# Kernel tuning notes

Hardware: AMD Instinct MI355X
Metric: run time of the kernel (lower is better)

Reference implementation:

```python
import jax, jax.numpy as jnp
import numpy as np
import math

FEATURE_DIM = 128
INPUT_DIM = 2
OUTPUT_DIM = 3
SIGMA_Q = 128.0
SIGMA_LS = [16.0, 64.0, 256.0]
N_PATCHES = 256
HIDDEN = 512
HEADS = 2
DIM_HEAD = 64
ALPHA = 10.0
N_FREQ = FEATURE_DIM // (2 * INPUT_DIM)  # 32
B, HW = 8, 16384


def _omegas(sigma):
    # torch.logspace(1, log10(sigma), n): 10^1 .. sigma, n points
    return jnp.logspace(1.0, math.log10(sigma), N_FREQ, dtype=jnp.float32)


def calc_gamma(coords, omegas):
    # coords: [L, D] -> [L, D*2*n]
    arg = jnp.pi * coords[:, :, None] * omegas[None, None, :]  # [L, D, n]
    g = jnp.concatenate([jnp.sin(arg), jnp.cos(arg)], axis=-1)  # [L, D, 2n]
    return g.reshape(coords.shape[0], -1)


def setup_inputs() -> dict:
    key = jax.random.key(0)
    ks = jax.random.split(key, 16)
    w = lambda k, shape: (jax.random.normal(k, shape, dtype=jnp.float32) * 0.05)
    return {
        "x": jax.random.uniform(ks[0], (B, HW, INPUT_DIM), dtype=jnp.float32),
        "tokens": jax.random.normal(ks[1], (B, N_PATCHES, HIDDEN), dtype=jnp.float32),
        "q_W": w(ks[2], (FEATURE_DIM, HIDDEN)),
        "q_b": w(ks[3], (HIDDEN,)),
        "Wq": w(ks[4], (HIDDEN, HEADS * DIM_HEAD)),
        "Wkv": w(ks[5], (HIDDEN, 2 * HEADS * DIM_HEAD)),
        "Wo": w(ks[6], (HEADS * DIM_HEAD, HIDDEN)),
        "bo": w(ks[7], (HIDDEN,)),
        "bw_W": w(ks[8], (3, FEATURE_DIM, HIDDEN)),
        "bw_b": w(ks[9], (3, HIDDEN)),
        "mod_W": w(ks[10], (3, HIDDEN, HIDDEN)),
        "mod_b": w(ks[11], (3, HIDDEN)),
        "hv_W": w(ks[12], (2, HIDDEN, HIDDEN)),
        "hv_b": w(ks[13], (2, HIDDEN)),
        "out_W": w(ks[14], (3, HIDDEN, OUTPUT_DIM)),
        "out_b": w(ks[15], (3, OUTPUT_DIM)),
    }


def reference(x, tokens, q_W, q_b, Wq, Wkv, Wo, bo, bw_W, bw_b, mod_W, mod_b,
              hv_W, hv_b, out_W, out_b):
    b, hw = x.shape[0], x.shape[1]
    grid = x[0]  # shared query grid [HW, 2]
    patch = int(math.sqrt(N_PATCHES))  # 16

    # relative-distance bias (ALiBi-like)
    row = (grid[:, 0] * patch).astype(jnp.int32)
    col = (grid[:, 1] * patch).astype(jnp.int32)
    idx = row * patch + col  # [HW]
    m = tokens.shape[1]
    t = idx.astype(jnp.float32) / (patch * patch)
    pos = (jnp.arange(m, dtype=jnp.float32) + 0.5) / m
    bias = -ALPHA * (t[:, None] - pos[None, :]) ** 2  # [HW, m]

    # query Fourier encode + linear
    xq = calc_gamma(grid, _omegas(SIGMA_Q))  # [HW, feature_dim]
    xq = jax.nn.relu(xq @ q_W + q_b)  # [HW, hidden]

    # shared-token cross attention (queries identical across batch)
    scale = DIM_HEAD ** -0.5
    q = (xq @ Wq).reshape(hw, HEADS, DIM_HEAD)  # [HW, H, Dh]
    kv = tokens @ Wkv  # [B, m, 2*H*Dh]
    k, v = jnp.split(kv, 2, axis=-1)
    k = k.reshape(b, m, HEADS, DIM_HEAD)
    v = v.reshape(b, m, HEADS, DIM_HEAD)
    sim = jnp.einsum('qhd,bkhd->bhqk', q, k) * scale + bias[None, None]
    attn = jax.nn.softmax(sim, axis=-1)
    out = jnp.einsum('bhqk,bkhd->bqhd', attn, v).reshape(b, hw, HEADS * DIM_HEAD)
    mod = out @ Wo + bo  # [B, HW, hidden] modulation vector

    # multi-band MLPs
    mods = []
    for i in range(len(SIGMA_LS)):
        gl = calc_gamma(grid, _omegas(SIGMA_LS[i]))  # [HW, feature_dim]
        h_l = jax.nn.relu(gl @ bw_W[i] + bw_b[i])  # [HW, hidden]
        m_l = jax.nn.relu(h_l[None] + mod @ mod_W[i] + mod_b[i])  # [B, HW, hidden]
        mods.append(m_l)

    h_v = mods[0]
    total = h_v @ out_W[0] + out_b[0]
    for i in range(len(SIGMA_LS) - 1):
        h_v = jax.nn.relu((mods[i + 1] + h_v) @ hv_W[i] + hv_b[i])
        total = total + h_v @ out_W[i + 1] + out_b[i + 1]

    return total.reshape(b, hw, -1)
```

## Files before the change

kernel.cpp:

```cpp
#include <hip/hip_runtime.h>
#include <math.h>

typedef unsigned short u16;
typedef unsigned int uint;
typedef __bf16 bf16x8 __attribute__((ext_vector_type(8)));
typedef unsigned short u16x8 __attribute__((ext_vector_type(8)));
typedef float f32x4 __attribute__((ext_vector_type(4)));

#define HWQ 16384
#define PI_F 3.14159265358979323846f

#define C_X     0
#define C_TOK   262144
#define C_QW    1310720
#define C_QB    1376256
#define C_WQ    1376768
#define C_WKV   1442304
#define C_WO    1704448
#define C_BO    1769984
#define C_BWW   1770496
#define C_BWB   1967104
#define C_MODW  1968640
#define C_MODB  2755072
#define C_HVW   2756608
#define C_HVB   3280896
#define C_OUTW  3281920
#define C_OUTB  3286528
#define C_TOTAL 3286537
#define CANON_PAD 3286544

#define QWT_OFF  0
#define WQT_OFF  65536
#define WOT_OFF  131072
#define BWT_OFF  196608
#define MODT_OFF 393216
#define HVT_OFF  1179648

struct SrcPtrs { const void* p[16]; };

__device__ __forceinline__ float bs2f(u16 u){
  unsigned v = ((unsigned)u) << 16; float f; __builtin_memcpy(&f, &v, 4); return f;
}
__device__ __forceinline__ u16 f2bs(float f){
  unsigned v; __builtin_memcpy(&v, &f, 4);
  v = (v + 0x7fffu + ((v >> 16) & 1u)) >> 16;
  return (u16)v;
}
__device__ __forceinline__ f32x4 mfma16(bf16x8 a, bf16x8 b, f32x4 c){
  return __builtin_amdgcn_mfma_f32_16x16x32_bf16(a, b, c, 0, 0, 0);
}
__device__ __forceinline__ bf16x8 ld8(const u16* p){ return *(const bf16x8*)p; }
__device__ __forceinline__ void ld2lds(const u16* g, u16* l){
  __builtin_amdgcn_global_load_lds((__attribute__((address_space(1))) const uint*)g,
                                   (__attribute__((address_space(3))) uint*)l, 16, 0, 0);
}

__global__ void k_detect(const u16* qb_raw, unsigned* flag){
  __shared__ int cnt[256];
  int t = threadIdx.x;
  u16 u = qb_raw[2*t];
  int e = (u >> 7) & 0xFF;
  cnt[t] = (e >= 126) ? 1 : 0;
  __syncthreads();
  for (int s = 128; s > 0; s >>= 1){
    if (t < s) cnt[t] += cnt[t + s];
    __syncthreads();
  }
  if (t == 0) *flag = (cnt[0] >= 16) ? 1u : 0u;
}

__global__ __launch_bounds__(256) void k_convert(SrcPtrs sp, const unsigned* flag, u16* canon){
  const int offs[17] = {C_X,C_TOK,C_QW,C_QB,C_WQ,C_WKV,C_WO,C_BO,C_BWW,C_BWB,
                        C_MODW,C_MODB,C_HVW,C_HVB,C_OUTW,C_OUTB,C_TOTAL};
  int e = blockIdx.x * 256 + threadIdx.x;
  if (e >= C_TOTAL) return;
  int seg = 0;
  for (int i = 1; i < 16; i++) if (e >= offs[i]) seg = i;
  int local = e - offs[seg];
  if (*flag) canon[e] = f2bs(((const float*)sp.p[seg])[local]);
  else       canon[e] = ((const u16*)sp.p[seg])[local];
}

__global__ __launch_bounds__(256) void k_tr(const u16* canon, u16* WT){
  __shared__ u16 tile[32][33];
  int bid = blockIdx.x, t = threadIdx.x;
  const u16* src; u16* dst; int K, N, tl;
  bool kblk = (bid >= 384);
  if (bid < 384){
    int m = bid >> 6; tl = bid & 63;
    if (m == 0){ src = canon + C_QW;  dst = WT + QWT_OFF; K = 128; N = 512; }
    else if (m == 1){ src = canon + C_WQ; dst = WT + WQT_OFF; K = 512; N = 128; }
    else if (m == 2){ src = canon + C_WO; dst = WT + WOT_OFF; K = 128; N = 512; }
    else { src = canon + C_BWW + (m-3)*65536; dst = WT + BWT_OFF + (m-3)*65536; K = 128; N = 512; }
  } else if (bid < 1152){
    int m = (bid - 384) >> 8; tl = (bid - 384) & 255;
    src = canon + C_MODW + m*262144; dst = WT + MODT_OFF + m*262144; K = 512; N = 512;
  } else {
    int m = (bid - 1152) >> 8; tl = (bid - 1152) & 255;
    src = canon + C_HVW + m*262144; dst = WT + HVT_OFF + m*262144; K = 512; N = 512;
  }
  int kt = K >> 5;
  int k0 = (tl % kt) * 32, n0 = (tl / kt) * 32;
  int tx = t & 31, ty = t >> 5;
  for (int r = 0; r < 4; r++)
    tile[ty + r*8][tx] = src[(size_t)(k0 + ty + r*8) * N + n0 + tx];
  __syncthreads();
  if (!kblk){
    for (int r = 0; r < 4; r++)
      dst[(size_t)(n0 + ty + r*8) * K + k0 + tx] = tile[tx][ty + r*8];
  } else {
    u16* d2 = dst + (size_t)(k0 >> 5)*16384;
    for (int r = 0; r < 4; r++)
      d2[(n0 + ty + r*8)*32 + tx] = tile[tx][ty + r*8];
  }
}

__global__ __launch_bounds__(256) void k_kv(const u16* canon, u16* kpart, u16* vT){
  int b = blockIdx.x >> 8, kk = blockIdx.x & 255, t = threadIdx.x;
  const u16* tok = canon + C_TOK;
  const u16* Wkv = canon + C_WKV;
  __shared__ float tk[512];
  const u16* tr = tok + ((size_t)(b*256 + kk)) * 512;
  tk[t] = bs2f(tr[t]); tk[t+256] = bs2f(tr[t+256]);
  __syncthreads();
  float acc = 0.f;
  for (int k = 0; k < 512; k++) acc += tk[k] * bs2f(Wkv[k*256 + t]);
  if (t < 128) kpart[((size_t)(b*256 + kk))*128 + t] = f2bs(acc);
  else vT[((size_t)b*128 + (t-128))*256 + kk] = f2bs(acc);
}

__global__ __launch_bounds__(256) void k_query(const u16* canon, const float* xraw,
      const unsigned* flag, const u16* WT, u16* qvecB, u16* hlB){
  int t = threadIdx.x, q0 = blockIdx.x * 16;
  const u16* q_b = canon + C_QB;
  const u16* bw_b= canon + C_BWB;
  int lane = t & 63, wv = t >> 6, l15 = lane & 15, q4 = lane >> 4;
  __shared__ __align__(16) u16 g[16*136];
  __shared__ __align__(16) u16 xql[16*520];
  __shared__ float cco[32];
  __shared__ float omg[32];
  for (int e = t; e < 16*136; e += 256) g[e] = 0;
  for (int e = t; e < 16*520; e += 256) xql[e] = 0;
  if (t < 32) cco[t] = (*flag) ? xraw[q0*2 + t] : bs2f(canon[C_X + q0*2 + t]);
  if (t < 32) omg[t] = (float)pow(10.0, 1.0 + t * ((2.1072099696478683 - 1.0)/31.0));
  __syncthreads();
  for (int i = 0; i < 8; i++){
    int id = i*256 + t, qi = id >> 7, f = id & 127;
    int d = f >> 6, r = f & 63, fi = r & 31;
    float arg = PI_F * cco[qi*2 + d] * omg[fi];
    g[qi*136 + f] = f2bs((r < 32) ? sinf(arg) : cosf(arg));
  }
  __syncthreads();
  {
    const u16* Bm = WT + QWT_OFF;
    for (int nt = 0; nt < 8; nt++){
      f32x4 acc = {0.f,0.f,0.f,0.f};
      int c = wv*128 + nt*16 + l15;
      for (int ks = 0; ks < 4; ks++){
        bf16x8 a  = ld8(g + l15*136 + ks*32 + q4*8);
        bf16x8 bb = ld8(Bm + (size_t)c*128 + ks*32 + q4*8);
        acc = mfma16(a, bb, acc);
      }
      float qb = bs2f(q_b[c]);
      for (int rg = 0; rg < 4; rg++){
        int row = q4*4 + rg;
        xql[row*520 + c] = f2bs(fmaxf(acc[rg] + qb, 0.f));
      }
    }
  }
  __syncthreads();
  {
    const u16* Bm = WT + WQT_OFF;
    for (int nh = 0; nh < 2; nh++){
      f32x4 acc = {0.f,0.f,0.f,0.f};
      int c = wv*32 + nh*16 + l15;
      for (int ks = 0; ks < 16; ks++){
        bf16x8 a  = ld8(xql + l15*520 + ks*32 + q4*8);
        bf16x8 bb = ld8(Bm + (size_t)c*512 + ks*32 + q4*8);
        acc = mfma16(a, bb, acc);
      }
      for (int rg = 0; rg < 4; rg++)
        g[(q4*4 + rg)*128 + c] = f2bs(acc[rg]);
    }
    __syncthreads();
    {
      int rr = t >> 4, cc = (t & 15)*8;
      *(u16x8*)(qvecB + (size_t)(q0 + rr)*128 + cc) = *(const u16x8*)(g + rr*128 + cc);
    }
  }
  const double LG[3] = {1.2041199826559248, 1.8061799739838869, 2.4082399653118496};
  for (int ib = 0; ib < 3; ib++){
    __syncthreads();
    if (t < 32) omg[t] = (float)pow(10.0, 1.0 + t * ((LG[ib] - 1.0)/31.0));
    __syncthreads();
    for (int i = 0; i < 8; i++){
      int id = i*256 + t, qi = id >> 7, f = id & 127;
      int d = f >> 6, r = f & 63, fi = r & 31;
      float arg = PI_F * cco[qi*2 + d] * omg[fi];
      g[qi*136 + f] = f2bs((r < 32) ? sinf(arg) : cosf(arg));
    }
    __syncthreads();
    const u16* Bm = WT + BWT_OFF + ib*65536;
    for (int nt = 0; nt < 8; nt++){
      f32x4 acc = {0.f,0.f,0.f,0.f};
      int c = wv*128 + nt*16 + l15;
      for (int ks = 0; ks < 4; ks++){
        bf16x8 a  = ld8(g + l15*136 + ks*32 + q4*8);
        bf16x8 bb = ld8(Bm + (size_t)c*128 + ks*32 + q4*8);
        acc = mfma16(a, bb, acc);
      }
      float bias = bs2f(bw_b[ib*512 + c]);
      for (int rg = 0; rg < 4; rg++)
        xql[(q4*4 + rg)*520 + c] = f2bs(fmaxf(acc[rg] + bias, 0.f));
    }
    __syncthreads();
    for (int it = 0; it < 4; it++){
      int rr = it*4 + (t >> 6), cc = (t & 63)*8;
      *(u16x8*)(hlB + ((size_t)ib*HWQ + q0 + rr)*512 + cc) = *(const u16x8*)(xql + rr*520 + cc);
    }
  }
}

__global__ __launch_bounds__(256) void k_attn(const u16* canon, const float* xraw,
      const unsigned* flag, const u16* qvecB, const u16* kpart, const u16* vT,
      const u16* WT, u16* modB){
  int t = threadIdx.x;
  int b = blockIdx.x & 7, qt = blockIdx.x >> 3, q0 = qt*32;
  const u16* bo = canon + C_BO;
  int lane = t & 63, wv = t >> 6, l15 = lane & 15, q4 = lane >> 4;
  __shared__ __align__(16) u16 ql[32*136];
  __shared__ __align__(16) u16 pl[32*264];
  __shared__ __align__(16) float pf[32*264];
  __shared__ __align__(16) u16 ot[32*136];
  __shared__ float tqs[32];
  __shared__ float red[256];
  __shared__ float rst[32];
  for (int e = t; e < 32*136; e += 256){ ql[e] = 0; ot[e] = 0; }
  for (int e = t; e < 32*264; e += 256) pl[e] = 0;
  __syncthreads();
  for (int i = 0; i < 16; i++){
    int id = i*256 + t, qi = id >> 7, c = id & 127;
    ql[qi*136 + c] = qvecB[(size_t)(q0 + qi)*128 + c];
  }
  if (t < 32){
    float c0, c1;
    if (*flag){ c0 = xraw[(q0+t)*2]; c1 = xraw[(q0+t)*2 + 1]; }
    else { c0 = bs2f(canon[C_X + (q0+t)*2]); c1 = bs2f(canon[C_X + (q0+t)*2 + 1]); }
    int rr = (int)(c0*16.f), cc = (int)(c1*16.f);
    tqs[t] = (float)(rr*16 + cc) * (1.f/256.f);
  }
  __syncthreads();
  for (int h = 0; h < 2; h++){
    f32x4 sac[2][4];
    for (int mt = 0; mt < 2; mt++) for (int nt = 0; nt < 4; nt++) sac[mt][nt] = (f32x4){0.f,0.f,0.f,0.f};
    const u16* kb = kpart + (size_t)b*256*128 + h*64;
    for (int ks = 0; ks < 2; ks++){
      bf16x8 a0 = ld8(ql + l15*136 + h*64 + ks*32 + q4*8);
      bf16x8 a1 = ld8(ql + (16+l15)*136 + h*64 + ks*32 + q4*8);
      for (int nt = 0; nt < 4; nt++){
        int kk = wv*64 + nt*16 + l15;
        bf16x8 bb = ld8(kb + (size_t)kk*128 + ks*32 + q4*8);
        sac[0][nt] = mfma16(a0, bb, sac[0][nt]);
        sac[1][nt] = mfma16(a1, bb, sac[1][nt]);
      }
    }
    for (int mt = 0; mt < 2; mt++) for (int nt = 0; nt < 4; nt++){
      int kk = wv*64 + nt*16 + l15;
      float pos = ((float)kk + 0.5f) * (1.f/256.f);
      for (int rg = 0; rg < 4; rg++){
        int row = mt*16 + q4*4 + rg;
        float dd = tqs[row] - pos;
        pf[row*264 + kk] = sac[mt][nt][rg]*0.125f - 10.f*dd*dd;
      }
    }
    __syncthreads();
    {
      int r = t >> 3, i = t & 7;
      float* pr = pf + r*264 + i*32;
      u16* po = pl + r*264 + i*32;
      float m = -1e30f;
      for (int j = 0; j < 32; j++) m = fmaxf(m, pr[j]);
      red[t] = m;
      __syncthreads();
      if (t < 32){ float mm = red[t*8];
        for (int j = 1; j < 8; j++) mm = fmaxf(mm, red[t*8+j]);
        rst[t] = mm; }
      __syncthreads();
      float mm = rst[r], sum = 0.f;
      for (int j = 0; j < 32; j++){ float e = expf(pr[j] - mm); pr[j] = e; sum += e; }
      red[t] = sum;
      __syncthreads();
      if (t < 32){ float ss = 0.f;
        for (int j = 0; j < 8; j++) ss += red[t*8+j];
        rst[t] = 1.f/ss; }
      __syncthreads();
      float inv = rst[r];
      for (int j = 0; j < 32; j++) po[j] = f2bs(pr[j] * inv);
    }
    __syncthreads();
    f32x4 oac[2] = {(f32x4){0.f,0.f,0.f,0.f}, (f32x4){0.f,0.f,0.f,0.f}};
    const u16* vb = vT + ((size_t)b*128 + h*64)*256;
    int dl = wv*16 + l15;
    for (int ks = 0; ks < 8; ks++){
      bf16x8 a0 = ld8(pl + l15*264 + ks*32 + q4*8);
      bf16x8 a1 = ld8(pl + (16+l15)*264 + ks*32 + q4*8);
      bf16x8 bb = ld8(vb + (size_t)dl*256 + ks*32 + q4*8);
      oac[0] = mfma16(a0, bb, oac[0]);
      oac[1] = mfma16(a1, bb, oac[1]);
    }
    for (int mt = 0; mt < 2; mt++) for (int rg = 0; rg < 4; rg++){
      int row = mt*16 + q4*4 + rg;
      ot[row*136 + h*64 + dl] = f2bs(oac[mt][rg]);
    }
    __syncthreads();
  }
  u16* stg = (u16*)pf;
  const u16* wob = WT + WOT_OFF;
  for (int nt = 0; nt < 8; nt++){
    f32x4 mac[2] = {(f32x4){0.f,0.f,0.f,0.f}, (f32x4){0.f,0.f,0.f,0.f}};
    int c = wv*128 + nt*16 + l15;
    for (int ks = 0; ks < 4; ks++){
      bf16x8 a0 = ld8(ot + l15*136 + ks*32 + q4*8);
      bf16x8 a1 = ld8(ot + (16+l15)*136 + ks*32 + q4*8);
      bf16x8 bb = ld8(wob + (size_t)c*128 + ks*32 + q4*8);
      mac[0] = mfma16(a0, bb, mac[0]);
      mac[1] = mfma16(a1, bb, mac[1]);
    }
    float bv = bs2f(bo[c]);
    for (int mt = 0; mt < 2; mt++) for (int rg = 0; rg < 4; rg++){
      int row = mt*16 + q4*4 + rg;
      stg[row*512 + c] = f2bs(mac[mt][rg] + bv);
    }
  }
  __syncthreads();
  for (int it = 0; it < 8; it++){
    int rr = it*4 + (t >> 6), cc = (t & 63)*8;
    int q = q0 + rr;
    int rgp = q >> 3, r = (q & 7)*8 + b;
    size_t off = (size_t)rgp*32768 + (size_t)(cc >> 5)*2048 + (size_t)(r >> 4)*512
               + (size_t)((cc >> 3) & 3)*128 + (size_t)(r & 15)*8;
    *(u16x8*)(modB + off) = *(const u16x8*)(stg + rr*512 + cc);
  }
}


#define ZACC2 for (int mt = 0; mt < 4; mt++) for (int nt = 0; nt < 4; nt++){ \
  accA[mt][nt] = (f32x4){0.f,0.f,0.f,0.f}; accB[mt][nt] = (f32x4){0.f,0.f,0.f,0.f}; }

#define XLI(row, c) (((c) >> 5)*2048 + (((row) >> 4))*512 + ((((c) >> 3) & 3))*128 + (((row) & 15))*8 + ((c) & 7))

#define MM16(ACC, A0,A1,A2,A3, B0,B1,B2,B3)                                      \
  ACC[0][0]=mfma16(A0,B0,ACC[0][0]); ACC[0][1]=mfma16(A0,B1,ACC[0][1]);          \
  ACC[0][2]=mfma16(A0,B2,ACC[0][2]); ACC[0][3]=mfma16(A0,B3,ACC[0][3]);          \
  ACC[1][0]=mfma16(A1,B0,ACC[1][0]); ACC[1][1]=mfma16(A1,B1,ACC[1][1]);          \
  ACC[1][2]=mfma16(A1,B2,ACC[1][2]); ACC[1][3]=mfma16(A1,B3,ACC[1][3]);          \
  ACC[2][0]=mfma16(A2,B0,ACC[2][0]); ACC[2][1]=mfma16(A2,B1,ACC[2][1]);          \
  ACC[2][2]=mfma16(A2,B2,ACC[2][2]); ACC[2][3]=mfma16(A2,B3,ACC[2][3]);          \
  ACC[3][0]=mfma16(A3,B0,ACC[3][0]); ACC[3][1]=mfma16(A3,B1,ACC[3][1]);          \
  ACC[3][2]=mfma16(A3,B2,ACC[3][2]); ACC[3][3]=mfma16(A3,B3,ACC[3][3]);

#define GEMM2A(Abuf, Bg0, Bg1)                                                   \
  { ZACC2                                                                        \
    const u16* b0p = (Bg0) + (size_t)(w*64 + l15)*32 + q4*8;                     \
    const u16* b1p = (Bg1) + (size_t)(w*64 + l15)*32 + q4*8;                     \
    const u16* ap  = (Abuf) + q4*128 + l15*8;                                    \
    _Pragma("unroll 1")                                                          \
    for (int ks = 0; ks < 16; ks++){                                             \
      bf16x8 u0=ld8(b0p+ks*16384), u1=ld8(b0p+ks*16384+512),                     \
             u2=ld8(b0p+ks*16384+1024), u3=ld8(b0p+ks*16384+1536);               \
      bf16x8 v0=ld8(b1p+ks*16384), v1=ld8(b1p+ks*16384+512),                     \
             v2=ld8(b1p+ks*16384+1024), v3=ld8(b1p+ks*16384+1536);               \
      bf16x8 a0=ld8(ap+ks*2048), a1=ld8(ap+ks*2048+512),                         \
             a2=ld8(ap+ks*2048+1024), a3=ld8(ap+ks*2048+1536);                   \
      MM16(accA, a0,a1,a2,a3, u0,u1,u2,u3)                                       \
      MM16(accB, a0,a1,a2,a3, v0,v1,v2,v3)                                       \
    } }

#define GEMM2B(Ab0, Bg0, Ab1, Bg1)                                               \
  { ZACC2                                                                        \
    const u16* b0p = (Bg0) + (size_t)(w*64 + l15)*32 + q4*8;                     \
    const u16* b1p = (Bg1) + (size_t)(w*64 + l15)*32 + q4*8;                     \
    const u16* a0p = (Ab0) + q4*128 + l15*8;                                     \
    const u16* a1p = (Ab1) + q4*128 + l15*8;                                     \
    _Pragma("unroll 1")                                                          \
    for (int ks = 0; ks < 16; ks++){                                             \
      bf16x8 u0=ld8(b0p+ks*16384), u1=ld8(b0p+ks*16384+512),                     \
             u2=ld8(b0p+ks*16384+1024), u3=ld8(b0p+ks*16384+1536);               \
      bf16x8 v0=ld8(b1p+ks*16384), v1=ld8(b1p+ks*16384+512),                     \
             v2=ld8(b1p+ks*16384+1024), v3=ld8(b1p+ks*16384+1536);               \
      bf16x8 x0=ld8(a0p+ks*2048), x1=ld8(a0p+ks*2048+512),                       \
             x2=ld8(a0p+ks*2048+1024), x3=ld8(a0p+ks*2048+1536);                 \
      bf16x8 y0=ld8(a1p+ks*2048), y1=ld8(a1p+ks*2048+512),                       \
             y2=ld8(a1p+ks*2048+1024), y3=ld8(a1p+ks*2048+1536);                 \
      MM16(accA, x0,x1,x2,x3, u0,u1,u2,u3)                                       \
      MM16(accB, y0,y1,y2,y3, v0,v1,v2,v3)                                       \
    } }

#define GEMMC(Abuf, Bgl)                                                         \
  { for (int mt = 0; mt < 4; mt++) for (int nt = 0; nt < 4; nt++)                \
      accA[mt][nt] = (f32x4){0.f,0.f,0.f,0.f};                                   \
    const u16* bptr = (Bgl) + (size_t)(w*64 + l15)*32 + q4*8;                    \
    const u16* ap   = (Abuf) + q4*128 + l15*8;                                   \
    _Pragma("unroll 1")                                                          \
    for (int ks = 0; ks < 16; ks++){                                             \
      bf16x8 u0=ld8(bptr+ks*16384), u1=ld8(bptr+ks*16384+512),                   \
             u2=ld8(bptr+ks*16384+1024), u3=ld8(bptr+ks*16384+1536);             \
      bf16x8 a0=ld8(ap+ks*2048), a1=ld8(ap+ks*2048+512),                         \
             a2=ld8(ap+ks*2048+1024), a3=ld8(ap+ks*2048+1536);                   \
      MM16(accA, a0,a1,a2,a3, u0,u1,u2,u3)                                       \
    } }

#define PROJ_REDUCE                                                              \
  __syncthreads();                                                               \
  if (t < 192){ float s = 0.f;                                                   \
    for (int w2 = 0; w2 < 8; w2++) s += pscr[w2*192 + t];                        \
    totrow[t] += s; }                                                            \
  __syncthreads();

__global__ __launch_bounds__(512, 2) void k_bands3(const u16* canon, const u16* modB,
      const u16* WT, const u16* hlB, const unsigned* flag, void* outv){
  int t = threadIdx.x, rgp = blockIdx.x;
  int lane = t & 63, w = t >> 6, l15 = lane & 15, q4 = lane >> 4;
  __shared__ __align__(16) u16 XL[16*64*32];
  __shared__ __align__(16) u16 AL[16*64*32];
  __shared__ float pscr[1536];
  __shared__ float totrow[192];
  if (t < 192){
    int o = t - (t/3)*3;
    totrow[t] = bs2f(canon[C_OUTB + o]) + bs2f(canon[C_OUTB + 3 + o]) + bs2f(canon[C_OUTB + 6 + o]);
  }
  {
    const u16* src = modB + (size_t)rgp*32768;
    for (int i = 0; i < 8; i++)
      ld2lds(src + i*4096 + w*512 + lane*8, AL + i*4096 + w*512);
  }
  const u16* hl0 = hlB;
  const u16* hl1 = hlB + (size_t)HWQ*512;
  const u16* hl2 = hlB + (size_t)2*HWQ*512;
  int qbase = rgp*8;
  f32x4 accA[4][4], accB[4][4];
  __syncthreads();

  GEMM2A(AL, WT + MODT_OFF, WT + MODT_OFF + 262144);
  {
    float ow[4][3], b0v[4], b1v[4];
    for (int nt = 0; nt < 4; nt++){
      int c = w*64 + nt*16 + l15;
      b0v[nt] = bs2f(canon[C_MODB + c]);
      b1v[nt] = bs2f(canon[C_MODB + 512 + c]);
      for (int o = 0; o < 3; o++) ow[nt][o] = bs2f(canon[C_OUTW + c*3 + o]);
    }
    for (int mt = 0; mt < 4; mt++) for (int rg = 0; rg < 4; rg++){
      int row = mt*16 + q4*4 + rg;
      int q = qbase + (row >> 3);
      float p0 = 0.f, p1 = 0.f, p2 = 0.f;
      for (int nt = 0; nt < 4; nt++){
        int c = w*64 + nt*16 + l15;
        float v1 = accA[mt][nt][rg] + b0v[nt] + bs2f(hl0[(size_t)q*512 + c]);
        v1 = fmaxf(v1, 0.f);
        float v2 = accB[mt][nt][rg] + b1v[nt] + bs2f(hl1[(size_t)q*512 + c]);
        v2 = fmaxf(v2, 0.f) + v1;
        XL[XLI(row, c)] = f2bs(v2);
        p0 += v1*ow[nt][0]; p1 += v1*ow[nt][1]; p2 += v1*ow[nt][2];
      }
      for (int m = 1; m < 16; m <<= 1){
        p0 += __shfl_xor(p0, m, 64); p1 += __shfl_xor(p1, m, 64); p2 += __shfl_xor(p2, m, 64);
      }
      if (l15 == 0){
        pscr[w*192 + row*3 + 0] = p0;
        pscr[w*192 + row*3 + 1] = p1;
        pscr[w*192 + row*3 + 2] = p2;
      }
    }
  }
  PROJ_REDUCE;

  GEMM2B(XL, WT + HVT_OFF, AL, WT + MODT_OFF + 524288);
  __syncthreads();
  {
    float ow[4][3], hb[4], b2v[4];
    for (int nt = 0; nt < 4; nt++){
      int c = w*64 + nt*16 + l15;
      hb[nt]  = bs2f(canon[C_HVB + c]);
      b2v[nt] = bs2f(canon[C_MODB + 1024 + c]);
      for (int o = 0; o < 3; o++) ow[nt][o] = bs2f(canon[C_OUTW + 1536 + c*3 + o]);
    }
    for (int mt = 0; mt < 4; mt++) for (int rg = 0; rg < 4; rg++){
      int row = mt*16 + q4*4 + rg;
      int q = qbase + (row >> 3);
      float p0 = 0.f, p1 = 0.f, p2 = 0.f;
      for (int nt = 0; nt < 4; nt++){
        int c = w*64 + nt*16 + l15;
        float v3 = fmaxf(accA[mt][nt][rg] + hb[nt], 0.f);
        float v4 = accB[mt][nt][rg] + b2v[nt] + bs2f(hl2[(size_t)q*512 + c]);
        v4 = fmaxf(v4, 0.f) + v3;
        XL[XLI(row, c)] = f2bs(v4);
        p0 += v3*ow[nt][0]; p1 += v3*ow[nt][1]; p2 += v3*ow[nt][2];
      }
      for (int m = 1; m < 16; m <<= 1){
        p0 += __shfl_xor(p0, m, 64); p1 += __shfl_xor(p1, m, 64); p2 += __shfl_xor(p2, m, 64);
      }
      if (l15 == 0){
        pscr[w*192 + row*3 + 0] = p0;
        pscr[w*192 + row*3 + 1] = p1;
        pscr[w*192 + row*3 + 2] = p2;
      }
    }
  }
  PROJ_REDUCE;

  GEMMC(XL, WT + HVT_OFF + 262144);
  {
    float ow[4][3], hb[4];
    for (int nt = 0; nt < 4; nt++){
      int c = w*64 + nt*16 + l15;
      hb[nt] = bs2f(canon[C_HVB + 512 + c]);
      for (int o = 0; o < 3; o++) ow[nt][o] = bs2f(canon[C_OUTW + 3072 + c*3 + o]);
    }
    for (int mt = 0; mt < 4; mt++) for (int rg = 0; rg < 4; rg++){
      int row = mt*16 + q4*4 + rg;
      float p0 = 0.f, p1 = 0.f, p2 = 0.f;
      for (int nt = 0; nt < 4; nt++){
        float v = fmaxf(accA[mt][nt][rg] + hb[nt], 0.f);
        p0 += v*ow[nt][0]; p1 += v*ow[nt][1]; p2 += v*ow[nt][2];
      }
      for (int m = 1; m < 16; m <<= 1){
        p0 += __shfl_xor(p0, m, 64); p1 += __shfl_xor(p1, m, 64); p2 += __shfl_xor(p2, m, 64);
      }
      if (l15 == 0){
        pscr[w*192 + row*3 + 0] = p0;
        pscr[w*192 + row*3 + 1] = p1;
        pscr[w*192 + row*3 + 2] = p2;
      }
    }
  }
  PROJ_REDUCE;

  if (t < 192){
    int row = t / 3, o = t - (t/3)*3;
    int gr = rgp*64 + row;
    int b = gr & 7, q = gr >> 3;
    size_t idx = ((size_t)b*HWQ + q)*3 + o;
    if (*flag) ((float*)outv)[idx] = totrow[t];
    else       ((u16*)outv)[idx]   = f2bs(totrow[t]);
  }
}

extern "C" void kernel_launch(void* const* d_in, const int* in_sizes, int n_in,
                              void* d_out, int out_size, void* d_ws, size_t ws_size,
                              hipStream_t stream){
  (void)in_sizes; (void)n_in; (void)out_size;

  u16* wsp   = (u16*)d_ws;
  unsigned* flag = (unsigned*)wsp;
  u16* canon = wsp + 8;
  u16* WT    = canon + CANON_PAD;
  u16* kpart = WT + 1703936;
  u16* vT    = kpart + 262144;
  u16* qvecB = vT + 262144;
  u16* hlB   = qvecB + 2097152;
  u16* modB  = hlB + 25165824;
  if (ws_size < 199773250ULL) return;

  SrcPtrs sp;
  for (int i = 0; i < 16; i++) sp.p[i] = d_in[i];
  const float* xraw = (const float*)d_in[0];

  k_detect <<<1, 256, 0, stream>>>((const u16*)d_in[3], flag);
  k_convert<<<(C_TOTAL + 255)/256, 256, 0, stream>>>(sp, flag, canon);
  k_tr     <<<1664, 256, 0, stream>>>(canon, WT);
  k_kv     <<<2048, 256, 0, stream>>>(canon, kpart, vT);
  k_query  <<<1024, 256, 0, stream>>>(canon, xraw, flag, WT, qvecB, hlB);
  k_attn   <<<4096, 256, 0, stream>>>(canon, xraw, flag, qvecB, kpart, vT, WT, modB);
  k_bands3 <<<2048, 512, 0, stream>>>(canon, modB, WT, hlB, flag, d_out);
}
```

Baseline: 910.1 us.

## Compute attention softmax in registers with wavefront shuffles and deferred normalization

The attention kernel keeps scores in the MFMA accumulator registers instead of writing an fp32 score tile to shared memory. Row max and row sum now come from cross-lane shuffles plus a small per-wave shared reduction, replacing the serial per-thread scans and several barriers. Normalization moves to the PV output, scaling by the inverse sum before the bf16 store. Dropping the fp32 buffer and the zero-fill loops also cuts shared-memory use, at the cost of more live registers.

```diff
diff --git a/kernel.cpp b/kernel.cpp
--- a/kernel.cpp
+++ b/kernel.cpp
@@ -229,15 +229,11 @@
   const u16* bo = canon + C_BO;
   int lane = t & 63, wv = t >> 6, l15 = lane & 15, q4 = lane >> 4;
   __shared__ __align__(16) u16 ql[32*136];
-  __shared__ __align__(16) u16 pl[32*264];
-  __shared__ __align__(16) float pf[32*264];
+  __shared__ __align__(16) u16 sbuf[32*512];
   __shared__ __align__(16) u16 ot[32*136];
   __shared__ float tqs[32];
-  __shared__ float red[256];
-  __shared__ float rst[32];
-  for (int e = t; e < 32*136; e += 256){ ql[e] = 0; ot[e] = 0; }
-  for (int e = t; e < 32*264; e += 256) pl[e] = 0;
-  __syncthreads();
+  __shared__ float rred [128];
+  __shared__ float rred2[128];
   for (int i = 0; i < 16; i++){
     int id = i*256 + t, qi = id >> 7, c = id & 127;
     ql[qi*136 + c] = qvecB[(size_t)(q0 + qi)*128 + c];
@@ -250,6 +246,7 @@
     tqs[t] = (float)(rr*16 + cc) * (1.f/256.f);
   }
   __syncthreads();
+  u16* pl = sbuf;
   for (int h = 0; h < 2; h++){
     f32x4 sac[2][4];
     for (int mt = 0; mt < 2; mt++) for (int nt = 0; nt < 4; nt++) sac[mt][nt] = (f32x4){0.f,0.f,0.f,0.f};
@@ -264,40 +261,56 @@
         sac[1][nt] = mfma16(a1, bb, sac[1][nt]);
       }
     }
+    float pmax[8];
+    for (int i = 0; i < 8; i++) pmax[i] = -1e30f;
     for (int mt = 0; mt < 2; mt++) for (int nt = 0; nt < 4; nt++){
       int kk = wv*64 + nt*16 + l15;
       float pos = ((float)kk + 0.5f) * (1.f/256.f);
       for (int rg = 0; rg < 4; rg++){
         int row = mt*16 + q4*4 + rg;
         float dd = tqs[row] - pos;
-        pf[row*264 + kk] = sac[mt][nt][rg]*0.125f - 10.f*dd*dd;
-      }
-    }
-    __syncthreads();
-    {
-      int r = t >> 3, i = t & 7;
-      float* pr = pf + r*264 + i*32;
-      u16* po = pl + r*264 + i*32;
-      float m = -1e30f;
-      for (int j = 0; j < 32; j++) m = fmaxf(m, pr[j]);
-      red[t] = m;
-      __syncthreads();
-      if (t < 32){ float mm = red[t*8];
-        for (int j = 1; j < 8; j++) mm = fmaxf(mm, red[t*8+j]);
-        rst[t] = mm; }
-      __syncthreads();
-      float mm = rst[r], sum = 0.f;
-      for (int j = 0; j < 32; j++){ float e = expf(pr[j] - mm); pr[j] = e; sum += e; }
-      red[t] = sum;
-      __syncthreads();
-      if (t < 32){ float ss = 0.f;
-        for (int j = 0; j < 8; j++) ss += red[t*8+j];
-        rst[t] = 1.f/ss; }
-      __syncthreads();
-      float inv = rst[r];
-      for (int j = 0; j < 32; j++) po[j] = f2bs(pr[j] * inv);
-    }
-    __syncthreads();
+        float s = sac[mt][nt][rg]*0.125f - 10.f*dd*dd;
+        sac[mt][nt][rg] = s;
+        pmax[mt*4+rg] = fmaxf(pmax[mt*4+rg], s);
+      }
+    }
+    for (int m = 1; m < 16; m <<= 1)
+      for (int i = 0; i < 8; i++) pmax[i] = fmaxf(pmax[i], __shfl_xor(pmax[i], m, 64));
+    if (l15 == 0)
+      for (int i = 0; i < 8; i++){
+        int row = (i>>2)*16 + q4*4 + (i&3);
+        rred[wv*32 + row] = pmax[i];
+      }
+    __syncthreads();
+    float gmax[8];
+    for (int i = 0; i < 8; i++){
+      int row = (i>>2)*16 + q4*4 + (i&3);
+      gmax[i] = fmaxf(fmaxf(rred[row], rred[32+row]), fmaxf(rred[64+row], rred[96+row]));
+    }
+    float psum[8];
+    for (int i = 0; i < 8; i++) psum[i] = 0.f;
+    for (int mt = 0; mt < 2; mt++) for (int nt = 0; nt < 4; nt++){
+      int kk = wv*64 + nt*16 + l15;
+      for (int rg = 0; rg < 4; rg++){
+        int row = mt*16 + q4*4 + rg;
+        float e = expf(sac[mt][nt][rg] - gmax[mt*4+rg]);
+        pl[row*264 + kk] = f2bs(e);
+        psum[mt*4+rg] += e;
+      }
+    }
+    for (int m = 1; m < 16; m <<= 1)
+      for (int i = 0; i < 8; i++) psum[i] += __shfl_xor(psum[i], m, 64);
+    if (l15 == 0)
+      for (int i = 0; i < 8; i++){
+        int row = (i>>2)*16 + q4*4 + (i&3);
+        rred2[wv*32 + row] = psum[i];
+      }
+    __syncthreads();
+    float inv[8];
+    for (int i = 0; i < 8; i++){
+      int row = (i>>2)*16 + q4*4 + (i&3);
+      inv[i] = 1.f/(rred2[row] + rred2[32+row] + rred2[64+row] + rred2[96+row]);
+    }
     f32x4 oac[2] = {(f32x4){0.f,0.f,0.f,0.f}, (f32x4){0.f,0.f,0.f,0.f}};
     const u16* vb = vT + ((size_t)b*128 + h*64)*256;
     int dl = wv*16 + l15;
@@ -310,11 +323,11 @@
     }
     for (int mt = 0; mt < 2; mt++) for (int rg = 0; rg < 4; rg++){
       int row = mt*16 + q4*4 + rg;
-      ot[row*136 + h*64 + dl] = f2bs(oac[mt][rg]);
-    }
-    __syncthreads();
-  }
-  u16* stg = (u16*)pf;
+      ot[row*136 + h*64 + dl] = f2bs(oac[mt][rg] * inv[mt*4+rg]);
+    }
+  }
+  __syncthreads();
+  u16* stg = sbuf;
   const u16* wob = WT + WOT_OFF;
   for (int nt = 0; nt < 8; nt++){
     f32x4 mac[2] = {(f32x4){0.f,0.f,0.f,0.f}, (f32x4){0.f,0.f,0.f,0.f}};
@@ -342,7 +355,6 @@
     *(u16x8*)(modB + off) = *(const u16x8*)(stg + rr*512 + cc);
   }
 }
-
 
 #define ZACC2 for (int mt = 0; mt < 4; mt++) for (int nt = 0; nt < 4; nt++){ \
   accA[mt][nt] = (f32x4){0.f,0.f,0.f,0.f}; accB[mt][nt] = (f32x4){0.f,0.f,0.f,0.f}; }
```

Result: faster. 868.9 us (-4.5%).
